# Kernel optimization log

Measured on AMD Instinct MI355X. Metric: run time of the kernel, lower is better.

The kernel has to match this reference:

```python
import jax, jax.numpy as jnp
import numpy as np

B, L, D = 2, 2048, 2048        # batch, seqlen, d_model
DIN, N, R, K = 4096, 16, 128, 4  # d_inner, d_state, dt_rank, d_conv


def setup_inputs() -> dict:
    key = jax.random.key(0)
    ks = jax.random.split(key, 9)
    hidden_states = jax.random.normal(ks[0], (B, L, D), dtype=jnp.float32) * 0.02
    in_proj_w = jax.random.normal(ks[1], (2 * DIN, D), dtype=jnp.float32) * (1.0 / np.sqrt(D))
    conv1d_w = jax.random.normal(ks[2], (DIN, K), dtype=jnp.float32) * (1.0 / np.sqrt(DIN))
    x_proj_w = jax.random.normal(ks[3], (R + 2 * N, DIN), dtype=jnp.float32) * (1.0 / np.sqrt(DIN))
    dt_proj_w = jax.random.normal(ks[4], (DIN, R), dtype=jnp.float32) * (1.0 / np.sqrt(R))
    # dt_proj_bias init: inverse-softplus of dt ~ LogUniform(1e-3, 1e-1), as in init_dtprojbias
    dt = jnp.exp(jax.random.uniform(ks[5], (DIN,)) * (np.log(0.1) - np.log(0.001)) + np.log(0.001))
    dt = jnp.clip(dt, 1e-4, None)
    dt_proj_bias = dt + jnp.log(-jnp.expm1(-dt))
    # A_log init: log(arange(1..N)) broadcast over d_inner (init_A)
    A_log = jnp.broadcast_to(jnp.log(jnp.arange(1, N + 1, dtype=jnp.float32)), (DIN, N))
    D_param = jnp.ones((DIN,), dtype=jnp.float32)
    out_proj_w = jax.random.normal(ks[6], (D, DIN), dtype=jnp.float32) * (1.0 / np.sqrt(DIN))
    return {
        "hidden_states": hidden_states, "in_proj_w": in_proj_w, "conv1d_w": conv1d_w,
        "x_proj_w": x_proj_w, "dt_proj_w": dt_proj_w, "dt_proj_bias": dt_proj_bias,
        "A_log": A_log, "D_param": D_param, "out_proj_w": out_proj_w,
    }


def _mamba_forward(hidden_states, in_proj_w, conv1d_w, x_proj_w, dt_proj_w,
                   dt_proj_bias, A_log, D_param, out_proj_w):
    b, l, _ = hidden_states.shape
    # in_proj: (b,l,d_model) -> (b,l,2*d_inner), split into x and gate z
    xz = jnp.einsum("bld,ed->ble", hidden_states, in_proj_w)
    x, z = jnp.split(xz, 2, axis=-1)  # each (b,l,d_inner)

    # depthwise causal conv1d along l, no bias, then SiLU
    xp = jnp.pad(x, ((0, 0), (K - 1, 0), (0, 0)))
    xc = sum(conv1d_w[:, k] * xp[:, k:k + l, :] for k in range(K))  # (b,l,d_inner)
    xc = jax.nn.silu(xc)

    # x_proj -> dt_rank + 2*d_state, split into dt, B, C
    x_dbl = jnp.einsum("bld,ed->ble", xc, x_proj_w)
    dt_r = x_dbl[..., :R]                    # (b,l,R)
    Bc = x_dbl[..., R:R + N]                 # (b,l,N)
    Cc = x_dbl[..., R + N:]                  # (b,l,N)
    delta = jax.nn.softplus(jnp.einsum("blr,dr->bld", dt_r, dt_proj_w) + dt_proj_bias)  # (b,l,d_inner)

    A = -jnp.exp(A_log)  # (d_inner, N)

    # selective scan: h_t = exp(delta_t*A)*h_{t-1} + delta_t*x_t*B_t; y_t = <h_t, C_t>
    def step(h, inp):
        delta_t, B_t, C_t, x_t = inp  # (b,d), (b,n), (b,n), (b,d)
        dA = jnp.exp(delta_t[..., None] * A)                 # (b,d,n)
        h = h * dA + (delta_t * x_t)[..., None] * B_t[:, None, :]
        y_t = jnp.einsum("bdn,bn->bd", h, C_t)
        return h, y_t

    inputs = (jnp.swapaxes(delta, 0, 1), jnp.swapaxes(Bc, 0, 1),
              jnp.swapaxes(Cc, 0, 1), jnp.swapaxes(xc, 0, 1))
    h0 = jnp.zeros((b, DIN, N), dtype=xc.dtype)
    _, y = jax.lax.scan(step, h0, inputs)     # y: (l,b,d_inner)
    y = jnp.swapaxes(y, 0, 1)                 # (b,l,d_inner)

    y = y + xc * D_param                      # skip term
    y = y * jax.nn.silu(z)                    # gating
    return jnp.einsum("bld,ed->ble", y, out_proj_w)  # (b,l,d_model)


def reference(hidden_states, in_proj_w, conv1d_w, x_proj_w, dt_proj_w,
              dt_proj_bias, A_log, D_param, out_proj_w):
    return _mamba_forward(hidden_states, in_proj_w, conv1d_w, x_proj_w, dt_proj_w,
                          dt_proj_bias, A_log, D_param, out_proj_w)
```

## Files before the change

### kernel.cpp

```cpp
#include <hip/hip_runtime.h>
#include <math.h>

#define DIN   4096
#define NST   16
#define RR    128
#define LSEQ  2048
#define NTOK  4096
#define BB    2
#define CHUNK 64
#define NCH   (LSEQ / CHUNK)
#define KSPL  8
#define KC    (DIN / KSPL)

typedef __attribute__((ext_vector_type(8))) short short8;
typedef __attribute__((ext_vector_type(4))) float f32x4;

__device__ __forceinline__ float sigmoidf_(float x) { return 1.f / (1.f + __expf(-x)); }
__device__ __forceinline__ float softplusf_(float x) {
    return fmaxf(x, 0.f) + log1pf(__expf(-fabsf(x)));
}
__device__ __forceinline__ unsigned short f2bf_(float f) {
    unsigned u = __float_as_uint(f);
    return (unsigned short)((u + 0x7FFFu + ((u >> 16) & 1u)) >> 16);
}
__device__ __forceinline__ void gld_lds16_(const unsigned short* g, unsigned short* l) {
    __builtin_amdgcn_global_load_lds((const __attribute__((address_space(1))) unsigned int*)g,
                                     (__attribute__((address_space(3))) unsigned int*)l,
                                     16, 0, 0);
}

__global__ __launch_bounds__(256)
void f2bf_kernel(const float* __restrict__ src, unsigned short* __restrict__ dst, int n8)
{
    int i = blockIdx.x * 256 + threadIdx.x;
    if (i >= n8) return;
    const float4* s = (const float4*)src + 2 * (size_t)i;
    float4 a = s[0], b = s[1];
    union { unsigned short u[8]; uint4 v; } o;
    o.u[0] = f2bf_(a.x); o.u[1] = f2bf_(a.y); o.u[2] = f2bf_(a.z); o.u[3] = f2bf_(a.w);
    o.u[4] = f2bf_(b.x); o.u[5] = f2bf_(b.y); o.u[6] = f2bf_(b.z); o.u[7] = f2bf_(b.w);
    ((uint4*)dst)[i] = o.v;
}

__global__ __launch_bounds__(256)
void add_f4_kernel(float* __restrict__ dst, const float* __restrict__ src, int n4)
{
    int i = blockIdx.x * 256 + threadIdx.x;
    if (i >= n4) return;
    float4 a = ((const float4*)dst)[i];
    float4 b = ((const float4*)src)[i];
    a.x += b.x; a.y += b.y; a.z += b.z; a.w += b.w;
    ((float4*)dst)[i] = a;
}


#define BAR()        asm volatile("s_barrier" ::: "memory")
#define WAIT_LGKM0() asm volatile("s_waitcnt lgkmcnt(0)" ::: "memory")
#define WAIT_VM(n)   asm volatile("s_waitcnt vmcnt(" #n ")" ::: "memory")


#define RD_A(P, mh) do { _Pragma("unroll") \
  for (int ii = 0; ii < 4; ++ii) { \
      aF[ii][0] = *(const short8*)((P) + (mh)*8192 + ii*2048 + co0); \
      aF[ii][1] = *(const short8*)((P) + (mh)*8192 + ii*2048 + co1); } } while (0)

#define RD_B(P, nh, DST) do { _Pragma("unroll") \
  for (int jj = 0; jj < 2; ++jj) { \
      DST[jj][0] = *(const short8*)((P) + (nh)*4096 + jj*2048 + co0); \
      DST[jj][1] = *(const short8*)((P) + (nh)*4096 + jj*2048 + co1); } } while (0)

#define MFMA_Q(mh, nh, BF) do { __builtin_amdgcn_s_setprio(1); _Pragma("unroll") \
  for (int ii = 0; ii < 4; ++ii) { _Pragma("unroll") \
    for (int jj = 0; jj < 2; ++jj) { _Pragma("unroll") \
      for (int ks = 0; ks < 2; ++ks) \
        acc[(mh)*4+ii][(nh)*2+jj] = __builtin_amdgcn_mfma_f32_16x16x32_bf16( \
            aF[ii][ks], BF[jj][ks], acc[(mh)*4+ii][(nh)*2+jj], 0, 0, 0); } } \
  __builtin_amdgcn_s_setprio(0); } while (0)

#define STGLD(gbase, sbase, h, l, tile) \
  gld_lds16_(gbase + (size_t)((h)*128 + (l)*64) * K + (size_t)(tile)*64, \
             (unsigned short*)(sbase + (h)*16384 + (l)*8192))

#define ITER(t, PREF) do { \
   \
  STGLD(gA0, sA1, 1, 0, (t)+1); STGLD(gA0, sA1, 1, 1, (t)+1); \
  BAR(); WAIT_LGKM0(); MFMA_Q(0, 0, bA); \
  RD_B(pB0c, 1, bB);                     \
  BAR(); \
   \
  BAR(); WAIT_LGKM0(); MFMA_Q(0, 1, bB); \
  RD_A(pA0, 1);                          \
  BAR(); \
   \
  if (PREF) { STGLD(gB0, sB0, 0, 0, (t)+2); STGLD(gB0, sB0, 0, 1, (t)+2); } \
  BAR(); WAIT_LGKM0(); MFMA_Q(1, 1, bB); \
  BAR(); \
   \
  if (PREF) { STGLD(gA0, sA0, 0, 0, (t)+2); STGLD(gA0, sA0, 0, 1, (t)+2); \
              STGLD(gB0, sB0, 1, 0, (t)+2); STGLD(gB0, sB0, 1, 1, (t)+2); } \
  BAR(); WAIT_LGKM0(); MFMA_Q(1, 0, bA); \
  if (PREF) { WAIT_VM(6); } else { WAIT_VM(0); } \
  RD_A(pA1, 0); RD_B(pB1c, 0, bA);       \
  BAR(); \
   \
  if (PREF) { STGLD(gA0, sA0, 1, 0, (t)+2); STGLD(gA0, sA0, 1, 1, (t)+2); } \
  BAR(); WAIT_LGKM0(); MFMA_Q(0, 0, bA); \
  RD_B(pB1c, 1, bB);                     \
  BAR(); \
   \
  BAR(); WAIT_LGKM0(); MFMA_Q(0, 1, bB); \
  RD_A(pA1, 1);                          \
  BAR(); \
   \
  if (PREF) { STGLD(gB0, sB1, 0, 0, (t)+3); STGLD(gB0, sB1, 0, 1, (t)+3); } \
  BAR(); WAIT_LGKM0(); MFMA_Q(1, 1, bB); \
  BAR(); \
   \
  if (PREF) { STGLD(gA0, sA1, 0, 0, (t)+3); STGLD(gA0, sA1, 0, 1, (t)+3); \
              STGLD(gB0, sB1, 1, 0, (t)+3); STGLD(gB0, sB1, 1, 1, (t)+3); } \
  BAR(); WAIT_LGKM0(); MFMA_Q(1, 0, bA); \
  if (PREF) { WAIT_VM(6); } else { WAIT_VM(0); } \
  if (PREF) { RD_A(pA0, 0); RD_B(pB0c, 0, bA); } \
  BAR(); \
} while (0)

template<int MODE>
__global__ __launch_bounds__(512)
void gemm256(const unsigned short* __restrict__ A, const unsigned short* __restrict__ W,
             float* __restrict__ C, int K, int KL, int ldc, float* __restrict__ C2,
             int nbx, int fx)
{
    __shared__ __align__(16) unsigned short sm[65536];
    char* smb = (char*)sm;

    const int tid = threadIdx.x;
    const int ln  = tid & 63;
    const int wv  = tid >> 6;
    const int wm  = wv >> 2;
    const int wn  = wv & 3;
    const int m15 = ln & 15;
    const int q   = ln >> 4;

    const int bid = blockIdx.x;
    const int xcd = bid & 7;
    const int idx = bid >> 3;
    const int cw  = nbx / fx;
    const int chh = (gridDim.x >> 3) / cw;
    const int bn_i = (xcd % fx) * cw  + idx % cw;
    int bm_i = (xcd / fx) * chh + idx / cw;
    int kh = 0;
    if (MODE == 3) { kh = bm_i >> 4; bm_i &= 15; }
    const int bm  = bm_i << 8;
    const int bn  = bn_i << 8;

    const int co0 = (q * 16) ^ ((m15 & 7) << 4);
    const int co1 = co0 ^ 64;
    const int ra_base = wm * 16384 + m15 * 128;
    const int rb_base = wn * 8192  + m15 * 128;
    const char* pA0  = smb + ra_base;
    const char* pA1  = smb + 65536 + ra_base;
    const char* pB0c = smb + 32768 + rb_base;
    const char* pB1c = smb + 98304 + rb_base;

    char* sA0 = smb +          tid * 16;
    char* sB0 = smb + 32768  + tid * 16;
    char* sA1 = smb + 65536  + tid * 16;
    char* sB1 = smb + 98304  + tid * 16;
    const int srow  = tid >> 3;
    const int secol = (((tid & 7) ^ ((tid >> 3) & 7)) * 8);
    const unsigned short* gA0 = A + (size_t)(bm + srow) * K + secol + (size_t)kh * KL;
    const unsigned short* gB0 = W + (size_t)(bn + srow) * K + secol + (size_t)kh * KL;

    f32x4  acc[8][4] = {};
    short8 aF[4][2], bA[2][2], bB[2][2];

    const int KT = KL >> 6;

    STGLD(gA0, sA0, 0, 0, 0); STGLD(gA0, sA0, 0, 1, 0);
    STGLD(gA0, sA0, 1, 0, 0); STGLD(gA0, sA0, 1, 1, 0);
    STGLD(gB0, sB0, 0, 0, 0); STGLD(gB0, sB0, 0, 1, 0);
    STGLD(gB0, sB0, 1, 0, 0); STGLD(gB0, sB0, 1, 1, 0);
    STGLD(gA0, sA1, 0, 0, 1); STGLD(gA0, sA1, 0, 1, 1);
    STGLD(gB0, sB1, 0, 0, 1); STGLD(gB0, sB1, 0, 1, 1);
    STGLD(gB0, sB1, 1, 0, 1); STGLD(gB0, sB1, 1, 1, 1);
    WAIT_VM(6);
    BAR();
    RD_A(pA0, 0); RD_B(pB0c, 0, bA);

    for (int t = 0; t < KT - 2; t += 2) ITER(t, 1);
    ITER(KT - 2, 0);

    float* Cp = C;
    int bcol = bn;
    if (MODE == 2 && bcol >= DIN) { Cp = C2; bcol -= DIN; }
    if (MODE == 3 && kh) Cp = C2;
    #pragma unroll
    for (int i = 0; i < 8; ++i) {
        int row = bm + wm * 128 + i * 16 + q * 4;
        #pragma unroll
        for (int j = 0; j < 4; ++j) {
            int col = bcol + wn * 64 + j * 16 + m15;
            #pragma unroll
            for (int r = 0; r < 4; ++r)
                Cp[(size_t)(row + r) * ldc + col] = acc[i][j][r];
        }
    }
}

template<int MODE>
__global__ __launch_bounds__(256)
void gemm_mfma_bt(const unsigned short* __restrict__ A, const unsigned short* __restrict__ W,
                  float* __restrict__ C, int K, int ldc,
                  const float* __restrict__ bias, float* __restrict__ C2)
{
    __shared__ unsigned short As[128 * 32];
    __shared__ unsigned short Ws[128 * 32];
    const int tid = threadIdx.x;
    const int bm = blockIdx.y << 7;
    int bn = blockIdx.x << 7;

    const int c0 = tid, c1 = tid + 256;
    const unsigned short* ga0 = A + (size_t)(bm + (c0 >> 2)) * K + (c0 & 3) * 8;
    const unsigned short* ga1 = A + (size_t)(bm + (c1 >> 2)) * K + (c1 & 3) * 8;
    const unsigned short* gw0 = W + (size_t)(bn + (c0 >> 2)) * K + (c0 & 3) * 8;
    const unsigned short* gw1 = W + (size_t)(bn + (c1 >> 2)) * K + (c1 & 3) * 8;
    unsigned short* la0 = &As[c0 * 8];
    unsigned short* la1 = &As[c1 * 8];
    unsigned short* lw0 = &Ws[c0 * 8];
    unsigned short* lw1 = &Ws[c1 * 8];

    const int ln  = tid & 63;
    const int wv  = tid >> 6;
    const int wm  = (wv >> 1) << 6;
    const int wn  = (wv & 1) << 6;
    const int m15 = ln & 15;
    const int q   = ln >> 4;

    f32x4 acc[4][4] = {};

    for (int k0 = 0; k0 < K; k0 += 32) {
        __syncthreads();
        gld_lds16_(ga0, la0); gld_lds16_(ga1, la1);
        gld_lds16_(gw0, lw0); gld_lds16_(gw1, lw1);
        ga0 += 32; ga1 += 32; gw0 += 32; gw1 += 32;
        __syncthreads();
        short8 af[4], wf[4];
        #pragma unroll
        for (int i = 0; i < 4; ++i)
            af[i] = *(const short8*)&As[(wm + i * 16 + m15) * 32 + q * 8];
        #pragma unroll
        for (int j = 0; j < 4; ++j)
            wf[j] = *(const short8*)&Ws[(wn + j * 16 + m15) * 32 + q * 8];
        #pragma unroll
        for (int i = 0; i < 4; ++i)
            #pragma unroll
            for (int j = 0; j < 4; ++j)
                acc[i][j] = __builtin_amdgcn_mfma_f32_16x16x32_bf16(af[i], wf[j],
                                                                    acc[i][j], 0, 0, 0);
    }

    float* Cp = C;
    if (MODE == 2 && bn >= DIN) { Cp = C2; bn -= DIN; }

    #pragma unroll
    for (int i = 0; i < 4; ++i)
        #pragma unroll
        for (int j = 0; j < 4; ++j) {
            int col = bn + wn + j * 16 + m15;
            #pragma unroll
            for (int r = 0; r < 4; ++r) {
                int row = bm + wm + i * 16 + q * 4 + r;
                float v = acc[i][j][r];
                if (MODE == 1) v = softplusf_(v + bias[col]);
                Cp[(size_t)row * ldc + col] = v;
            }
        }
}

__global__ __launch_bounds__(256)
void gemm_kspl_kernel(const float* __restrict__ A, const float* __restrict__ W,
                      float* __restrict__ partial)
{
    __shared__ float As[16][66];
    __shared__ float Ws[16][162];
    const int tid = threadIdx.x;
    const int tx = tid & 15;
    const int ty = tid >> 4;
    const int bm = blockIdx.x << 6;
    const int k0 = blockIdx.y * KC;

    float acc[4][10] = {};

    for (int kt = 0; kt < KC; kt += 16) {
        float2 a2[2];
        #pragma unroll
        for (int i = 0; i < 2; ++i) {
            int idx = tid + 256 * i;
            int row = idx >> 3, kofs = (idx & 7) * 2;
            a2[i] = *(const float2*)&A[(size_t)(bm + row) * DIN + k0 + kt + kofs];
        }
        float2 w2[5];
        #pragma unroll
        for (int i = 0; i < 5; ++i) {
            int idx = tid + 256 * i;
            int wrow = idx >> 3, wk = (idx & 7) * 2;
            w2[i] = *(const float2*)&W[(size_t)wrow * DIN + k0 + kt + wk];
        }
        __syncthreads();
        #pragma unroll
        for (int i = 0; i < 2; ++i) {
            int idx = tid + 256 * i;
            int row = idx >> 3, kofs = (idx & 7) * 2;
            As[kofs][row] = a2[i].x; As[kofs + 1][row] = a2[i].y;
        }
        #pragma unroll
        for (int i = 0; i < 5; ++i) {
            int idx = tid + 256 * i;
            int wrow = idx >> 3, wk = (idx & 7) * 2;
            Ws[wk][wrow] = w2[i].x; Ws[wk + 1][wrow] = w2[i].y;
        }
        __syncthreads();
        #pragma unroll
        for (int kk = 0; kk < 16; ++kk) {
            float2 av0 = *(const float2*)&As[kk][ty * 4];
            float2 av1 = *(const float2*)&As[kk][ty * 4 + 2];
            float a[4] = {av0.x, av0.y, av1.x, av1.y};
            float w[10];
            #pragma unroll
            for (int j = 0; j < 5; ++j) {
                float2 wv = *(const float2*)&Ws[kk][tx * 10 + 2 * j];
                w[2 * j] = wv.x; w[2 * j + 1] = wv.y;
            }
            #pragma unroll
            for (int i = 0; i < 4; ++i)
                #pragma unroll
                for (int j = 0; j < 10; ++j)
                    acc[i][j] = fmaf(a[i], w[j], acc[i][j]);
        }
        __syncthreads();
    }

    float* po = partial + (size_t)blockIdx.y * NTOK * 160;
    #pragma unroll
    for (int i = 0; i < 4; ++i) {
        int r = bm + ty * 4 + i;
        #pragma unroll
        for (int j = 0; j < 5; ++j)
            *(float2*)&po[(size_t)r * 160 + tx * 10 + 2 * j] =
                make_float2(acc[i][2 * j], acc[i][2 * j + 1]);
    }
}

__global__ __launch_bounds__(256)
void kspl_reduce_kernel(const float* __restrict__ partial, float* __restrict__ xdbl,
                        unsigned short* __restrict__ dtr)
{
    int idx = blockIdx.x * 256 + threadIdx.x;
    float s = 0.f;
    #pragma unroll
    for (int k = 0; k < KSPL; ++k)
        s += partial[(size_t)k * NTOK * 160 + idx];
    xdbl[idx] = s;
    int row = idx / 160;
    int col = idx - row * 160;
    if (col < RR) dtr[(size_t)row * RR + col] = f2bf_(s);
}

__global__ __launch_bounds__(256)
void conv_silu_kernel(const float* __restrict__ x, const float* __restrict__ cw,
                      float* __restrict__ xc)
{
    int idx = blockIdx.x * 256 + threadIdx.x;
    int d = idx & (DIN - 1);
    int tok = idx >> 12;
    int t = tok & (LSEQ - 1);
    float w0 = cw[d * 4 + 0], w1 = cw[d * 4 + 1];
    float w2 = cw[d * 4 + 2], w3 = cw[d * 4 + 3];
    const float* xp = x + (size_t)tok * DIN + d;
    float acc = w3 * xp[0];
    if (t >= 1) acc = fmaf(w2, xp[-DIN], acc);
    if (t >= 2) acc = fmaf(w1, xp[-2 * DIN], acc);
    if (t >= 3) acc = fmaf(w0, xp[-3 * DIN], acc);
    xc[idx] = acc * sigmoidf_(acc);
}

__global__ __launch_bounds__(256)
void scan_part1_kernel(const float* __restrict__ delta, const float* __restrict__ xc,
                       const float* __restrict__ xdbl, const float* __restrict__ A_log,
                       float* __restrict__ hloc, float* __restrict__ ssum)
{
    int d = blockIdx.x * 256 + threadIdx.x;
    int c = blockIdx.y;
    int b = blockIdx.z;
    float A[NST], h[NST];
    #pragma unroll
    for (int n = 0; n < NST; ++n) {
        A[n] = -__expf(A_log[d * NST + n]);
        h[n] = 0.f;
    }
    float s = 0.f;
    int tok = b * LSEQ + c * CHUNK;
    for (int t = 0; t < CHUNK; ++t, ++tok) {
        float dv = delta[(size_t)tok * DIN + d];
        float xv = xc[(size_t)tok * DIN + d];
        const float* bc = xdbl + (size_t)tok * 160 + RR;
        float dx = dv * xv;
        s += dv;
        #pragma unroll
        for (int n = 0; n < NST; ++n)
            h[n] = fmaf(h[n], __expf(dv * A[n]), dx * bc[n]);
    }
    size_t base = (size_t)(b * NCH + c) * NST * DIN + d;
    #pragma unroll
    for (int n = 0; n < NST; ++n) hloc[base + (size_t)n * DIN] = h[n];
    ssum[(size_t)(b * NCH + c) * DIN + d] = s;
}

__global__ __launch_bounds__(256)
void scan_part2_kernel(float* __restrict__ hloc, const float* __restrict__ ssum,
                       const float* __restrict__ A_log)
{
    int idx = blockIdx.x * 256 + threadIdx.x;
    int b = idx >> 12;
    int d = idx & (DIN - 1);
    float A[NST], hin[NST];
    #pragma unroll
    for (int n = 0; n < NST; ++n) {
        A[n] = -__expf(A_log[d * NST + n]);
        hin[n] = 0.f;
    }
    for (int c = 0; c < NCH; ++c) {
        size_t base = (size_t)(b * NCH + c) * NST * DIN + d;
        float s = ssum[(size_t)(b * NCH + c) * DIN + d];
        #pragma unroll
        for (int n = 0; n < NST; ++n) {
            float hl = hloc[base + (size_t)n * DIN];
            hloc[base + (size_t)n * DIN] = hin[n];
            hin[n] = fmaf(hin[n], __expf(A[n] * s), hl);
        }
    }
}

__global__ __launch_bounds__(256)
void scan_part3_kernel(const float* __restrict__ delta, float* __restrict__ xcy,
                       const float* __restrict__ xdbl, const float* __restrict__ z,
                       const float* __restrict__ A_log, const float* __restrict__ Dp,
                       const float* __restrict__ hin_buf)
{
    int d = blockIdx.x * 256 + threadIdx.x;
    int c = blockIdx.y;
    int b = blockIdx.z;
    float A[NST], h[NST];
    size_t base = (size_t)(b * NCH + c) * NST * DIN + d;
    #pragma unroll
    for (int n = 0; n < NST; ++n) {
        A[n] = -__expf(A_log[d * NST + n]);
        h[n] = hin_buf[base + (size_t)n * DIN];
    }
    float Dv = Dp[d];
    int tok = b * LSEQ + c * CHUNK;
    for (int t = 0; t < CHUNK; ++t, ++tok) {
        float dv = delta[(size_t)tok * DIN + d];
        float xv = xcy[(size_t)tok * DIN + d];
        float zv = z[(size_t)tok * DIN + d];
        const float* bc = xdbl + (size_t)tok * 160 + RR;
        float dx = dv * xv;
        float y = 0.f;
        #pragma unroll
        for (int n = 0; n < NST; ++n) {
            h[n] = fmaf(h[n], __expf(dv * A[n]), dx * bc[n]);
            y = fmaf(h[n], bc[NST + n], y);
        }
        y = (y + xv * Dv) * (zv * sigmoidf_(zv));
        xcy[(size_t)tok * DIN + d] = y;
    }
}

extern "C" void kernel_launch(void* const* d_in, const int* in_sizes, int n_in,
                              void* d_out, int out_size, void* d_ws, size_t ws_size,
                              hipStream_t stream)
{
    const float* hidden     = (const float*)d_in[0];
    const float* in_proj_w  = (const float*)d_in[1];
    const float* conv_w     = (const float*)d_in[2];
    const float* x_proj_w   = (const float*)d_in[3];
    const float* dt_proj_w  = (const float*)d_in[4];
    const float* dt_bias    = (const float*)d_in[5];
    const float* A_log      = (const float*)d_in[6];
    const float* D_param    = (const float*)d_in[7];
    const float* out_proj_w = (const float*)d_in[8];
    float* out = (float*)d_out;

    const size_t BIG = (size_t)NTOK * DIN * sizeof(float);
    char* ws = (char*)d_ws;
    float* xbuf = (float*)(ws);
    float* xc   = (float*)(ws + BIG);
    float* zbuf = (float*)(ws + 2 * BIG);
    float* xdbl = (float*)(ws + 3 * BIG);
    float* delta = xbuf;

    unsigned short* w_in_bf  = (unsigned short*)xc;
    unsigned short* hid_bf   = (unsigned short*)out;
    unsigned short* y_bf     = (unsigned short*)xbuf;
    unsigned short* w_out_bf = (unsigned short*)zbuf;

    float* xpart = out;
    unsigned short* dtr_bf = (unsigned short*)(out + (size_t)KSPL * NTOK * 160);
    unsigned short* dtw_bf = dtr_bf + (size_t)NTOK * RR;
    float* hloc  = out;
    float* ssum  = out + (size_t)BB * NCH * NST * DIN;

    f2bf_kernel<<<8192, 256, 0, stream>>>(in_proj_w, w_in_bf, (2 * DIN * 2048) / 8);
    f2bf_kernel<<<4096, 256, 0, stream>>>(hidden, hid_bf, (NTOK * 2048) / 8);
    gemm256<2><<<512, 512, 0, stream>>>(hid_bf, w_in_bf, xbuf, 2048, 2048, DIN,
                                        zbuf, 32, 4);
    conv_silu_kernel<<<(NTOK * DIN) / 256, 256, 0, stream>>>(xbuf, conv_w, xc);
    gemm_kspl_kernel<<<dim3(NTOK / 64, KSPL), 256, 0, stream>>>(xc, x_proj_w, xpart);
    kspl_reduce_kernel<<<(NTOK * 160) / 256, 256, 0, stream>>>(xpart, xdbl, dtr_bf);
    f2bf_kernel<<<256, 256, 0, stream>>>(dt_proj_w, dtw_bf, (DIN * RR) / 8);
    gemm_mfma_bt<1><<<dim3(32, 32), 256, 0, stream>>>(dtr_bf, dtw_bf, delta,
                                                      RR, DIN, dt_bias, nullptr);
    scan_part1_kernel<<<dim3(DIN / 256, NCH, BB), 256, 0, stream>>>(delta, xc, xdbl,
                                                                    A_log, hloc, ssum);
    scan_part2_kernel<<<(BB * DIN) / 256, 256, 0, stream>>>(hloc, ssum, A_log);
    scan_part3_kernel<<<dim3(DIN / 256, NCH, BB), 256, 0, stream>>>(delta, xc, xdbl,
                                                                    zbuf, A_log, D_param, hloc);
    f2bf_kernel<<<8192, 256, 0, stream>>>(xc, y_bf, (NTOK * DIN) / 8);
    f2bf_kernel<<<4096, 256, 0, stream>>>(out_proj_w, w_out_bf, (2048 * DIN) / 8);
    gemm256<3><<<256, 512, 0, stream>>>(y_bf, w_out_bf, out, 4096, 2048, 2048,
                                        xc, 8, 2);
    add_f4_kernel<<<8192, 256, 0, stream>>>(out, xc, (NTOK * 2048) / 4);
}
```

Baseline: 740.7 us.

## Load full LDS tile fragments up front and drop interleaved lgkm waits

```diff
diff --git a/kernel.cpp b/kernel.cpp
--- a/kernel.cpp
+++ b/kernel.cpp
@@ -55,26 +55,35 @@
 
 
 #define BAR()        asm volatile("s_barrier" ::: "memory")
-#define WAIT_LGKM0() asm volatile("s_waitcnt lgkmcnt(0)" ::: "memory")
 #define WAIT_VM(n)   asm volatile("s_waitcnt vmcnt(" #n ")" ::: "memory")
 
 
-#define RD_A(P, mh) do { _Pragma("unroll") \
+#define RD_A0(P) do { _Pragma("unroll") \
   for (int ii = 0; ii < 4; ++ii) { \
-      aF[ii][0] = *(const short8*)((P) + (mh)*8192 + ii*2048 + co0); \
-      aF[ii][1] = *(const short8*)((P) + (mh)*8192 + ii*2048 + co1); } } while (0)
-
-#define RD_B(P, nh, DST) do { _Pragma("unroll") \
+      aF[ii][0] = *(const short8*)((P) + ii*2048 + co0); \
+      aF[ii][1] = *(const short8*)((P) + ii*2048 + co1); } } while (0)
+
+#define RD_A1(P) do { _Pragma("unroll") \
+  for (int ii = 0; ii < 4; ++ii) { \
+      aG[ii][0] = *(const short8*)((P) + 8192 + ii*2048 + co0); \
+      aG[ii][1] = *(const short8*)((P) + 8192 + ii*2048 + co1); } } while (0)
+
+#define RD_B0(P) do { _Pragma("unroll") \
   for (int jj = 0; jj < 2; ++jj) { \
-      DST[jj][0] = *(const short8*)((P) + (nh)*4096 + jj*2048 + co0); \
-      DST[jj][1] = *(const short8*)((P) + (nh)*4096 + jj*2048 + co1); } } while (0)
-
-#define MFMA_Q(mh, nh, BF) do { __builtin_amdgcn_s_setprio(1); _Pragma("unroll") \
+      bA[jj][0] = *(const short8*)((P) + jj*2048 + co0); \
+      bA[jj][1] = *(const short8*)((P) + jj*2048 + co1); } } while (0)
+
+#define RD_B1(P) do { _Pragma("unroll") \
+  for (int jj = 0; jj < 2; ++jj) { \
+      bB[jj][0] = *(const short8*)((P) + 4096 + jj*2048 + co0); \
+      bB[jj][1] = *(const short8*)((P) + 4096 + jj*2048 + co1); } } while (0)
+
+#define MFMA_Q(AF, mh, BF, nh) do { __builtin_amdgcn_s_setprio(1); _Pragma("unroll") \
   for (int ii = 0; ii < 4; ++ii) { _Pragma("unroll") \
     for (int jj = 0; jj < 2; ++jj) { _Pragma("unroll") \
       for (int ks = 0; ks < 2; ++ks) \
         acc[(mh)*4+ii][(nh)*2+jj] = __builtin_amdgcn_mfma_f32_16x16x32_bf16( \
-            aF[ii][ks], BF[jj][ks], acc[(mh)*4+ii][(nh)*2+jj], 0, 0, 0); } } \
+            AF[ii][ks], BF[jj][ks], acc[(mh)*4+ii][(nh)*2+jj], 0, 0, 0); } } \
   __builtin_amdgcn_s_setprio(0); } while (0)
 
 #define STGLD(gbase, sbase, h, l, tile) \
@@ -84,43 +93,39 @@
 #define ITER(t, PREF) do { \
    \
   STGLD(gA0, sA1, 1, 0, (t)+1); STGLD(gA0, sA1, 1, 1, (t)+1); \
-  BAR(); WAIT_LGKM0(); MFMA_Q(0, 0, bA); \
-  RD_B(pB0c, 1, bB);                     \
-  BAR(); \
-   \
-  BAR(); WAIT_LGKM0(); MFMA_Q(0, 1, bB); \
-  RD_A(pA0, 1);                          \
+  RD_A0(pA0); RD_B0(pB0c); RD_B1(pB0c); RD_A1(pA0); \
+  MFMA_Q(aF, 0, bA, 0); \
+  BAR(); \
+   \
+  MFMA_Q(aF, 0, bB, 1); \
   BAR(); \
    \
   if (PREF) { STGLD(gB0, sB0, 0, 0, (t)+2); STGLD(gB0, sB0, 0, 1, (t)+2); } \
-  BAR(); WAIT_LGKM0(); MFMA_Q(1, 1, bB); \
+  MFMA_Q(aG, 1, bB, 1); \
   BAR(); \
    \
   if (PREF) { STGLD(gA0, sA0, 0, 0, (t)+2); STGLD(gA0, sA0, 0, 1, (t)+2); \
               STGLD(gB0, sB0, 1, 0, (t)+2); STGLD(gB0, sB0, 1, 1, (t)+2); } \
-  BAR(); WAIT_LGKM0(); MFMA_Q(1, 0, bA); \
+  MFMA_Q(aG, 1, bA, 0); \
   if (PREF) { WAIT_VM(6); } else { WAIT_VM(0); } \
-  RD_A(pA1, 0); RD_B(pB1c, 0, bA);       \
   BAR(); \
    \
   if (PREF) { STGLD(gA0, sA0, 1, 0, (t)+2); STGLD(gA0, sA0, 1, 1, (t)+2); } \
-  BAR(); WAIT_LGKM0(); MFMA_Q(0, 0, bA); \
-  RD_B(pB1c, 1, bB);                     \
-  BAR(); \
-   \
-  BAR(); WAIT_LGKM0(); MFMA_Q(0, 1, bB); \
-  RD_A(pA1, 1);                          \
+  RD_A0(pA1); RD_B0(pB1c); RD_B1(pB1c); RD_A1(pA1); \
+  MFMA_Q(aF, 0, bA, 0); \
+  BAR(); \
+   \
+  MFMA_Q(aF, 0, bB, 1); \
   BAR(); \
    \
   if (PREF) { STGLD(gB0, sB1, 0, 0, (t)+3); STGLD(gB0, sB1, 0, 1, (t)+3); } \
-  BAR(); WAIT_LGKM0(); MFMA_Q(1, 1, bB); \
+  MFMA_Q(aG, 1, bB, 1); \
   BAR(); \
    \
   if (PREF) { STGLD(gA0, sA1, 0, 0, (t)+3); STGLD(gA0, sA1, 0, 1, (t)+3); \
               STGLD(gB0, sB1, 1, 0, (t)+3); STGLD(gB0, sB1, 1, 1, (t)+3); } \
-  BAR(); WAIT_LGKM0(); MFMA_Q(1, 0, bA); \
+  MFMA_Q(aG, 1, bA, 0); \
   if (PREF) { WAIT_VM(6); } else { WAIT_VM(0); } \
-  if (PREF) { RD_A(pA0, 0); RD_B(pB0c, 0, bA); } \
   BAR(); \
 } while (0)
 
@@ -172,7 +177,7 @@
     const unsigned short* gB0 = W + (size_t)(bn + srow) * K + secol + (size_t)kh * KL;
 
     f32x4  acc[8][4] = {};
-    short8 aF[4][2], bA[2][2], bB[2][2];
+    short8 aF[4][2], aG[4][2], bA[2][2], bB[2][2];
 
     const int KT = KL >> 6;
 
@@ -185,7 +190,6 @@
     STGLD(gB0, sB1, 1, 0, 1); STGLD(gB0, sB1, 1, 1, 1);
     WAIT_VM(6);
     BAR();
-    RD_A(pA0, 0); RD_B(pB0c, 0, bA);
 
     for (int t = 0; t < KT - 2; t += 2) ITER(t, 1);
     ITER(KT - 2, 0);
```

Result: slower. 903.6 us (+22.0%).

## Restructure GEMM main loop into four phases with paired MFMA quadrants

Applied to the files above, without the earlier changes.

```diff
diff --git a/kernel.cpp b/kernel.cpp
--- a/kernel.cpp
+++ b/kernel.cpp
@@ -83,44 +83,28 @@
 
 #define ITER(t, PREF) do { \
    \
+  RD_A(pA0, 0); RD_B(pB0c, 0, bA); RD_B(pB0c, 1, bB); \
   STGLD(gA0, sA1, 1, 0, (t)+1); STGLD(gA0, sA1, 1, 1, (t)+1); \
-  BAR(); WAIT_LGKM0(); MFMA_Q(0, 0, bA); \
-  RD_B(pB0c, 1, bB);                     \
+  BAR(); WAIT_LGKM0(); MFMA_Q(0, 0, bA); MFMA_Q(0, 1, bB); BAR(); \
+   \
+  RD_A(pA0, 1); \
+  if (PREF) { STGLD(gA0, sA0, 0, 0, (t)+2); STGLD(gA0, sA0, 0, 1, (t)+2); \
+              STGLD(gB0, sB0, 0, 0, (t)+2); STGLD(gB0, sB0, 0, 1, (t)+2); \
+              STGLD(gB0, sB0, 1, 0, (t)+2); STGLD(gB0, sB0, 1, 1, (t)+2); } \
+  BAR(); WAIT_LGKM0(); MFMA_Q(1, 1, bB); MFMA_Q(1, 0, bA); \
+  if (PREF) { WAIT_VM(6); } else { WAIT_VM(0); } \
   BAR(); \
    \
-  BAR(); WAIT_LGKM0(); MFMA_Q(0, 1, bB); \
-  RD_A(pA0, 1);                          \
-  BAR(); \
+  RD_A(pA1, 0); RD_B(pB1c, 0, bA); RD_B(pB1c, 1, bB); \
+  if (PREF) { STGLD(gA0, sA0, 1, 0, (t)+2); STGLD(gA0, sA0, 1, 1, (t)+2); } \
+  BAR(); WAIT_LGKM0(); MFMA_Q(0, 0, bA); MFMA_Q(0, 1, bB); BAR(); \
    \
-  if (PREF) { STGLD(gB0, sB0, 0, 0, (t)+2); STGLD(gB0, sB0, 0, 1, (t)+2); } \
-  BAR(); WAIT_LGKM0(); MFMA_Q(1, 1, bB); \
-  BAR(); \
-   \
-  if (PREF) { STGLD(gA0, sA0, 0, 0, (t)+2); STGLD(gA0, sA0, 0, 1, (t)+2); \
-              STGLD(gB0, sB0, 1, 0, (t)+2); STGLD(gB0, sB0, 1, 1, (t)+2); } \
-  BAR(); WAIT_LGKM0(); MFMA_Q(1, 0, bA); \
+  RD_A(pA1, 1); \
+  if (PREF) { STGLD(gA0, sA1, 0, 0, (t)+3); STGLD(gA0, sA1, 0, 1, (t)+3); \
+              STGLD(gB0, sB1, 0, 0, (t)+3); STGLD(gB0, sB1, 0, 1, (t)+3); \
+              STGLD(gB0, sB1, 1, 0, (t)+3); STGLD(gB0, sB1, 1, 1, (t)+3); } \
+  BAR(); WAIT_LGKM0(); MFMA_Q(1, 1, bB); MFMA_Q(1, 0, bA); \
   if (PREF) { WAIT_VM(6); } else { WAIT_VM(0); } \
-  RD_A(pA1, 0); RD_B(pB1c, 0, bA);       \
-  BAR(); \
-   \
-  if (PREF) { STGLD(gA0, sA0, 1, 0, (t)+2); STGLD(gA0, sA0, 1, 1, (t)+2); } \
-  BAR(); WAIT_LGKM0(); MFMA_Q(0, 0, bA); \
-  RD_B(pB1c, 1, bB);                     \
-  BAR(); \
-   \
-  BAR(); WAIT_LGKM0(); MFMA_Q(0, 1, bB); \
-  RD_A(pA1, 1);                          \
-  BAR(); \
-   \
-  if (PREF) { STGLD(gB0, sB1, 0, 0, (t)+3); STGLD(gB0, sB1, 0, 1, (t)+3); } \
-  BAR(); WAIT_LGKM0(); MFMA_Q(1, 1, bB); \
-  BAR(); \
-   \
-  if (PREF) { STGLD(gA0, sA1, 0, 0, (t)+3); STGLD(gA0, sA1, 0, 1, (t)+3); \
-              STGLD(gB0, sB1, 1, 0, (t)+3); STGLD(gB0, sB1, 1, 1, (t)+3); } \
-  BAR(); WAIT_LGKM0(); MFMA_Q(1, 0, bA); \
-  if (PREF) { WAIT_VM(6); } else { WAIT_VM(0); } \
-  if (PREF) { RD_A(pA0, 0); RD_B(pB0c, 0, bA); } \
   BAR(); \
 } while (0)
 
@@ -185,7 +169,6 @@
     STGLD(gB0, sB1, 1, 0, 1); STGLD(gB0, sB1, 1, 1, 1);
     WAIT_VM(6);
     BAR();
-    RD_A(pA0, 0); RD_B(pB0c, 0, bA);
 
     for (int t = 0; t < KT - 2; t += 2) ITER(t, 1);
     ITER(KT - 2, 0);
```

Measured after the change: 717.8 us. 3.1% less time.
